# Kernel optimization log

Measured on AMD Instinct MI355X. Metric: run time of the kernel, lower is better.

The kernel has to match this reference:

```python
import jax, jax.numpy as jnp
import numpy as np

GRID = 12  # sqrt(144), seq_len = 144 fixed by w_g shape


def _relative_position(n: int) -> jnp.ndarray:
    # grid cell centers for an n x n grid, flattened row-major -> (n*n,)
    idx = np.arange(n * n)
    row, col = idx // n, idx % n
    cx = (col + 0.5) / n  # (x_min + x_max)/2 with x_min=col/n, x_max=(col+1)/n
    cy = (row + 0.5) / n
    dx = cx[:, None] - cx[None, :]
    dy = cy[:, None] - cy[None, :]
    ax = np.sign(dx) * 0.5
    ay = np.sign(dy) * 0.5
    dx = np.abs(np.log(np.abs(dx) + 0.5))
    dy = np.abs(np.log(np.abs(dy) + 0.5))
    # cat along leading dim then permute(1,2,0) == stack last-dim in order (dx,dy,ax,ay)
    pos = np.stack([dx, dy, ax, ay], axis=-1).astype(np.float32)  # (S,S,4)
    return jnp.asarray(pos)


def setup_inputs() -> dict:
    key = jax.random.key(0)
    ks = jax.random.split(key, 9)
    B, S, D = 128, GRID * GRID, 1024
    sc = 1.0 / np.sqrt(D)
    return {
        "query": jax.random.normal(ks[0], (B, S, D), jnp.float32),
        "key": jax.random.normal(ks[1], (B, S, D), jnp.float32),
        "value": jax.random.normal(ks[2], (B, S, D), jnp.float32),
        "Wq": jax.random.normal(ks[3], (D, D), jnp.float32) * sc,
        "bq": jnp.zeros((D,), jnp.float32),
        "Wk": jax.random.normal(ks[4], (D, D), jnp.float32) * sc,
        "bk": jnp.zeros((D,), jnp.float32),
        "Wv": jax.random.normal(ks[5], (D, D), jnp.float32) * sc,
        "bv": jnp.zeros((D,), jnp.float32),
        "Wlin": jax.random.normal(ks[6], (D, 4), jnp.float32) * 0.5,
        "w_g": jax.random.normal(ks[7], (S, D, 1), jnp.float32) * sc,
    }


def reference(query, key, value, Wq, bq, Wk, bk, Wv, bv, Wlin, w_g):
    d_model = query.shape[-1]
    # QKV projections + ReLU activation (dropout is identity at eval)
    q = jax.nn.relu(jnp.einsum("bsd,ed->bse", query, Wq) + bq)
    k = jax.nn.relu(jnp.einsum("bsd,ed->bse", key, Wk) + bk)
    v = jax.nn.relu(jnp.einsum("bsd,ed->bse", value, Wv) + bv)
    # raw scores: (B, S, S)
    att = jnp.einsum("bsd,btd->bst", q, k) * (d_model ** -0.5)
    # relative-position bias: (S, S, 4) -> linear -> relu -> per-row w_g -> relu
    pos = _relative_position(GRID)
    rp = jax.nn.relu(jnp.einsum("stf,df->std", pos, Wlin))  # (S, S, D)
    rp = jax.nn.relu(jnp.einsum("std,sdo->sto", rp, w_g)[..., 0])  # (S, S)
    att = jax.nn.softmax(att + rp[None, :, :], axis=-1)
    return jnp.einsum("bst,btd->bsd", att, v)
```

## Files before the change

kernel.cpp:

```cpp
#include <hip/hip_runtime.h>
#include <hip/hip_fp16.h>

#define DEV __device__ __forceinline__

using half8 = __attribute__((ext_vector_type(8))) _Float16;
using half4 = __attribute__((ext_vector_type(4))) _Float16;
using f32x4 = __attribute__((ext_vector_type(4))) float;

DEV void gload_lds16(const void* g, void* l) {
  __builtin_amdgcn_global_load_lds((const __attribute__((address_space(1))) unsigned int*)g,
                                   (__attribute__((address_space(3))) unsigned int*)l,
                                   16, 0, 0);
}

DEV f32x4 mfma16x32(half8 a, half8 b, f32x4 c) {
  return __builtin_amdgcn_mfma_f32_16x16x32_f16(a, b, c, 0, 0, 0);
}

__global__ void conv3_f32_f16(const float* __restrict__ s0, const float* __restrict__ s1,
                              const float* __restrict__ s2, _Float16* __restrict__ d0,
                              _Float16* __restrict__ d1, _Float16* __restrict__ d2, int n) {
  const float* s = blockIdx.z == 0 ? s0 : (blockIdx.z == 1 ? s1 : s2);
  _Float16* d = blockIdx.z == 0 ? d0 : (blockIdx.z == 1 ? d1 : d2);
  int i = (blockIdx.x * 256 + threadIdx.x) * 8;
  if (i >= n) return;
  float4 a = *(const float4*)(s + i);
  float4 b = *(const float4*)(s + i + 4);
  half8 h;
  h[0] = (_Float16)a.x; h[1] = (_Float16)a.y; h[2] = (_Float16)a.z; h[3] = (_Float16)a.w;
  h[4] = (_Float16)b.x; h[5] = (_Float16)b.y; h[6] = (_Float16)b.z; h[7] = (_Float16)b.w;
  *(half8*)(d + i) = h;
}

__global__ void vt_pad_zero(_Float16* __restrict__ vt) {
  int i = blockIdx.x * 256 + threadIdx.x;
  _Float16* p = vt + (size_t)i * 160 + 144;
  *(half8*)p = (half8){};
  *(half8*)(p + 8) = (half8){};
}

__global__ __launch_bounds__(192) void rp_kernel(const float* __restrict__ Wlin,
                                                 const float* __restrict__ wg,
                                                 float* __restrict__ rp) {
  int s = blockIdx.x, t = threadIdx.x;
  if (t >= 144) return;
  int rs = s / 12, cs = s % 12, rt = t / 12, ct = t % 12;
  float dx = (cs - ct) / 12.f, dy = (rs - rt) / 12.f;
  float ax = (dx > 0.f) ? 0.5f : (dx < 0.f ? -0.5f : 0.f);
  float ay = (dy > 0.f) ? 0.5f : (dy < 0.f ? -0.5f : 0.f);
  float lx = fabsf(logf(fabsf(dx) + 0.5f));
  float ly = fabsf(logf(fabsf(dy) + 0.5f));
  float a0 = 0.f, a1 = 0.f, a2 = 0.f, a3 = 0.f;
  const float* wgs = wg + s * 1024;
  for (int d = 0; d < 1024; d += 4) {
#pragma unroll
    for (int u = 0; u < 4; ++u) {
      float4 w = *(const float4*)(Wlin + (d + u) * 4);
      float dot = lx * w.x + ly * w.y + ax * w.z + ay * w.w;
      dot = dot > 0.f ? dot : 0.f;
      float p = dot * wgs[d + u];
      if (u == 0) a0 += p; else if (u == 1) a1 += p; else if (u == 2) a2 += p; else a3 += p;
    }
  }
  float acc = (a0 + a1) + (a2 + a3);
  rp[s * 144 + t] = acc > 0.f ? acc : 0.f;
}

__global__ __launch_bounds__(256, 2) void gemm_proj(
    const _Float16* __restrict__ a0q, const _Float16* __restrict__ a1q,
    const _Float16* __restrict__ a2q, const _Float16* __restrict__ w0q,
    const _Float16* __restrict__ w1q, const _Float16* __restrict__ w2q,
    const float* __restrict__ bi0, const float* __restrict__ bi1,
    const float* __restrict__ bi2, _Float16* __restrict__ c0q,
    _Float16* __restrict__ c1q, _Float16* __restrict__ c2q,
    _Float16* __restrict__ vtp, int vtz) {
  const _Float16* A = blockIdx.z == 0 ? a0q : (blockIdx.z == 1 ? a1q : a2q);
  const _Float16* W = blockIdx.z == 0 ? w0q : (blockIdx.z == 1 ? w1q : w2q);
  const float* bias = blockIdx.z == 0 ? bi0 : (blockIdx.z == 1 ? bi1 : bi2);
  _Float16* C = blockIdx.z == 0 ? c0q : (blockIdx.z == 1 ? c1q : c2q);

  __shared__ __align__(16) char lds[73728];
  int tid = threadIdx.x, wid = tid >> 6, lane = tid & 63;
  int lin = blockIdx.y * 8 + blockIdx.x;
  int local = lin >> 3;
  int mt = (lin & 7) * 9 + (local >> 3), nt = local & 7;
  int m0 = mt * 256, n0 = nt * 128;

  int r4l = lane >> 2, c4 = lane & 3;
  int cg8 = ((c4 + (r4l >> 1)) & 3) * 8;
  int lr = lane & 15, lg = lane >> 4;
  int rdoff = lr * 64 + ((lg - (lr >> 1)) & 3) * 16;

  const _Float16* gp[6];
#pragma unroll
  for (int c = 0; c < 6; ++c) {
    int q = c * 4 + wid;
    gp[c] = (q < 16) ? A + (size_t)(m0 + q * 16 + r4l) * 1024 + cg8
                     : W + (size_t)(n0 + (q - 16) * 16 + r4l) * 1024 + cg8;
  }
  char *sl0 = lds, *sl1 = lds + 24576, *sl2 = lds + 49152;
  auto issue = [&](char* slot) {
#pragma unroll
    for (int c = 0; c < 6; ++c) { gload_lds16(gp[c], slot + (c * 4 + wid) * 1024); gp[c] += 32; }
  };
  issue(sl0);
  issue(sl1);
  f32x4 acc[8][4] = {};
  int abase = (wid >> 1) * 8192, bbase = 16384 + (wid & 1) * 4096;
  for (int t = 0; t < 32; ++t) {
    asm volatile("s_waitcnt vmcnt(6)" ::: "memory");
    __builtin_amdgcn_s_barrier();
    __builtin_amdgcn_sched_barrier(0);
    issue(sl2);
    half8 a[8], b[4];
#pragma unroll
    for (int i = 0; i < 8; ++i) a[i] = *(const half8*)(sl0 + abase + i * 1024 + rdoff);
#pragma unroll
    for (int j = 0; j < 4; ++j) b[j] = *(const half8*)(sl0 + bbase + j * 1024 + rdoff);
#pragma unroll
    for (int i = 0; i < 8; ++i)
#pragma unroll
      for (int j = 0; j < 4; ++j)
        acc[i][j] = mfma16x32(b[j], a[i], acc[i][j]);
    char* tmp = sl0; sl0 = sl1; sl1 = sl2; sl2 = tmp;
  }
  int wm = (wid >> 1) * 128, wn = (wid & 1) * 64;
  bool tov = (vtp != nullptr) && ((int)blockIdx.z == vtz);
#pragma unroll
  for (int i = 0; i < 8; ++i) {
    int row = m0 + wm + i * 16 + lr;
#pragma unroll
    for (int j = 0; j < 4; ++j) {
      int col = n0 + wn + j * 16 + lg * 4;
      float4 b4 = *(const float4*)(bias + col);
      half4 h;
      float v0 = acc[i][j][0] + b4.x; h[0] = (_Float16)(v0 > 0.f ? v0 : 0.f);
      float v1 = acc[i][j][1] + b4.y; h[1] = (_Float16)(v1 > 0.f ? v1 : 0.f);
      float v2 = acc[i][j][2] + b4.z; h[2] = (_Float16)(v2 > 0.f ? v2 : 0.f);
      float v3 = acc[i][j][3] + b4.w; h[3] = (_Float16)(v3 > 0.f ? v3 : 0.f);
      if (tov) {
        int bb = row / 144, ss = row - bb * 144;
        _Float16* vb = vtp + (size_t)(bb * 1024 + col) * 160 + ss;
        vb[0] = h[0]; vb[160] = h[1]; vb[320] = h[2]; vb[480] = h[3];
      } else {
        *(half4*)(C + (size_t)row * 1024 + col) = h;
      }
    }
  }
}

__global__ __launch_bounds__(256) void attn_kernel(const _Float16* __restrict__ q,
                                                   const _Float16* __restrict__ k,
                                                   const _Float16* __restrict__ vt,
                                                   const float* __restrict__ rp,
                                                   float* __restrict__ out) {
  __shared__ __align__(16) char lds[53248];
  float* sc = (float*)lds;
  _Float16* P = (_Float16*)(lds + 36864);
  float* sums = (float*)(lds + 52992);

  int tid = threadIdx.x, wid = tid >> 6, lane = tid & 63;
  int lin = blockIdx.y * 3 + blockIdx.x;
  int swz = (lin & 7) * 48 + (lin >> 3);
  int mt3 = swz % 3, b = swz / 3;
  int m0 = mt3 * 48;
  const int nstart_t[4] = {0, 3, 5, 7};
  const int ncnt_t[4]   = {3, 2, 2, 2};
  int ns = nstart_t[wid], nc = ncnt_t[wid];
  int r4l = lane >> 2, c4 = lane & 3;
  int cg8 = ((c4 + (r4l >> 1)) & 3) * 8;
  int lr = lane & 15, lg = lane >> 4;
  int rdoff = lr * 64 + ((lg - (lr >> 1)) & 3) * 16;

  {
    char *sl0 = lds, *sl1 = lds + 12288, *sl2 = lds + 24576;
    const _Float16* g1[3];
#pragma unroll
    for (int c = 0; c < 3; ++c) {
      int qq = c * 4 + wid;
      g1[c] = (qq < 3) ? q + (size_t)(b * 144 + m0 + qq * 16 + r4l) * 1024 + cg8
                       : k + (size_t)(b * 144 + (qq - 3) * 16 + r4l) * 1024 + cg8;
    }
    auto issue1 = [&](char* slot) {
#pragma unroll
      for (int c = 0; c < 3; ++c) {
        gload_lds16(g1[c], slot + (c * 4 + wid) * 1024);
        g1[c] += 32;
      }
    };
    issue1(sl0);
    issue1(sl1);
    f32x4 acc[3][3] = {};
    for (int t = 0; t < 32; ++t) {
      asm volatile("s_waitcnt vmcnt(3)" ::: "memory");
      __builtin_amdgcn_sched_barrier(0);
      __builtin_amdgcn_s_barrier();
      __builtin_amdgcn_sched_barrier(0);
      issue1(sl2);
      half8 af[3], bf[3];
#pragma unroll
      for (int i = 0; i < 3; ++i)
        af[i] = *(const half8*)(sl0 + i * 1024 + rdoff);
#pragma unroll
      for (int j = 0; j < 3; ++j)
        if (j < nc)
          bf[j] = *(const half8*)(sl0 + (3 + ns + j) * 1024 + rdoff);
#pragma unroll
      for (int i = 0; i < 3; ++i)
#pragma unroll
        for (int j = 0; j < 3; ++j)
          if (j < nc)
            acc[i][j] = mfma16x32(bf[j], af[i], acc[i][j]);
      char* tmp = sl0; sl0 = sl1; sl1 = sl2; sl2 = tmp;
    }
    asm volatile("s_waitcnt vmcnt(0)" ::: "memory");
    __syncthreads();
    const float scale = 0.03125f;
#pragma unroll
    for (int i = 0; i < 3; ++i) {
      int qrow = i * 16 + lr;
#pragma unroll
      for (int j = 0; j < 3; ++j)
        if (j < nc) {
          int kc0 = (ns + j) * 16 + lg * 4;
          float4 rr = *(const float4*)(rp + (m0 + qrow) * 144 + kc0);
          f32x4 vs;
          vs[0] = acc[i][j][0] * scale + rr.x;
          vs[1] = acc[i][j][1] * scale + rr.y;
          vs[2] = acc[i][j][2] * scale + rr.z;
          vs[3] = acc[i][j][3] * scale + rr.w;
          *(f32x4*)(sc + qrow * 152 + kc0) = vs;
        }
    }
  }
  __syncthreads();

  if (tid < 192) {
    int r = tid >> 2, qd = tid & 3;
    int cb = qd * 36;
    float m = -1e30f;
    for (int c2 = 0; c2 < 36; ++c2) m = fmaxf(m, sc[r * 152 + cb + c2]);
    m = fmaxf(m, __shfl_xor(m, 1));
    m = fmaxf(m, __shfl_xor(m, 2));
    float s = 0.f;
    for (int c2 = 0; c2 < 36; ++c2) {
      float e = __expf(sc[r * 152 + cb + c2] - m);
      s += e;
      P[r * 168 + cb + c2] = (_Float16)e;
    }
    s += __shfl_xor(s, 1);
    s += __shfl_xor(s, 2);
    if (qd == 0) sums[r] = s;
  }
  if (tid < 96) {
    int r = tid >> 1, c0 = 144 + (tid & 1) * 8;
    *(half8*)(P + r * 168 + c0) = (half8){};
  }
  __syncthreads();

  char *s0p = lds, *s1p = lds + 16384;
  auto issue2 = [&](int idx, char* slot) {
    int nn0 = (idx / 5) * 256, kk0 = (idx % 5) * 32;
#pragma unroll
    for (int c = 0; c < 4; ++c) {
      int ch = c * 4 + wid;
      gload_lds16(vt + (size_t)(b * 1024 + nn0 + ch * 16 + r4l) * 160 + kk0 + cg8,
                  slot + ch * 1024);
    }
  };
  issue2(0, s0p);
  f32x4 o[3][4] = {};
  for (int it = 0; it < 20; ++it) {
    asm volatile("s_waitcnt vmcnt(0)" ::: "memory");
    __builtin_amdgcn_sched_barrier(0);
    __builtin_amdgcn_s_barrier();
    __builtin_amdgcn_sched_barrier(0);
    issue2(it + 1, ((it + 1) & 1) ? s1p : s0p);
    char* sb = (it & 1) ? s1p : s0p;
    int k0 = (it % 5) * 32;
    half8 af[3], bf[4];
#pragma unroll
    for (int i = 0; i < 3; ++i)
      af[i] = *(const half8*)(P + (i * 16 + lr) * 168 + k0 + lg * 8);
#pragma unroll
    for (int j = 0; j < 4; ++j)
      bf[j] = *(const half8*)(sb + (wid * 4 + j) * 1024 + rdoff);
#pragma unroll
    for (int i = 0; i < 3; ++i)
#pragma unroll
      for (int j = 0; j < 4; ++j)
        o[i][j] = mfma16x32(bf[j], af[i], o[i][j]);
    if (it % 5 == 4) {
      int n0 = (it / 5) * 256;
#pragma unroll
      for (int i = 0; i < 3; ++i) {
        int row = i * 16 + lr;
        float inv = 1.f / sums[row];
#pragma unroll
        for (int j = 0; j < 4; ++j) {
          f32x4 vo;
          vo[0] = o[i][j][0] * inv; vo[1] = o[i][j][1] * inv;
          vo[2] = o[i][j][2] * inv; vo[3] = o[i][j][3] * inv;
          *(f32x4*)(out + (size_t)(b * 144 + m0 + row) * 1024 + n0 + wid * 64 + j * 16 + lg * 4) = vo;
          o[i][j] = (f32x4){};
        }
      }
    }
  }
}

extern "C" void kernel_launch(void* const* d_in, const int* in_sizes, int n_in,
                              void* d_out, int out_size, void* d_ws, size_t ws_size,
                              hipStream_t stream) {
  const float* query = (const float*)d_in[0];
  const float* key   = (const float*)d_in[1];
  const float* value = (const float*)d_in[2];
  const float* Wq    = (const float*)d_in[3];
  const float* bq    = (const float*)d_in[4];
  const float* Wk    = (const float*)d_in[5];
  const float* bk    = (const float*)d_in[6];
  const float* Wv    = (const float*)d_in[7];
  const float* bv    = (const float*)d_in[8];
  const float* Wlin  = (const float*)d_in[9];
  const float* wg    = (const float*)d_in[10];
  float* out = (float*)d_out;

  char* ws = (char*)d_ws;
  const size_t NQKV = (size_t)18432 * 1024;
  const size_t NVT  = (size_t)131072 * 160;
  const int    NW   = 1024 * 1024;
  _Float16* Wqb = (_Float16*)(ws);
  _Float16* Wkb = (_Float16*)(ws + (2u << 20));
  _Float16* Wvb = (_Float16*)(ws + (4u << 20));
  float*    rp  = (float*)(ws + (6u << 20));
  _Float16* qp  = (_Float16*)(ws + (6u << 20) + 131072);
  _Float16* kp  = qp + NQKV;
  _Float16* vt  = kp + NQKV;

  dim3 agrid(3, 128);

  if (ws_size >= 238000000ull) {
    _Float16* ia = vt + NVT + 32768;
    _Float16* ib = ia + NQKV;
    _Float16* ic = ib + NQKV;
    conv3_f32_f16<<<dim3((int)(NQKV / 2048), 1, 3), 256, 0, stream>>>(
        query, key, value, ia, ib, ic, (int)NQKV);
    conv3_f32_f16<<<dim3(NW / 2048, 1, 3), 256, 0, stream>>>(Wq, Wk, Wv, Wqb, Wkb, Wvb, NW);
    rp_kernel<<<144, 192, 0, stream>>>(Wlin, wg, rp);
    vt_pad_zero<<<512, 256, 0, stream>>>(vt);
    gemm_proj<<<dim3(8, 72, 3), 256, 0, stream>>>(ia, ib, ic, Wqb, Wkb, Wvb,
                                                  bq, bk, bv, qp, kp, kp ,
                                                  vt, 2);
    attn_kernel<<<agrid, 256, 0, stream>>>(qp, kp, vt, rp, out);
  } else {
    _Float16* inb = vt + NVT;
    rp_kernel<<<144, 192, 0, stream>>>(Wlin, wg, rp);
    vt_pad_zero<<<512, 256, 0, stream>>>(vt);
    conv3_f32_f16<<<dim3(NW / 2048, 1, 3), 256, 0, stream>>>(Wq, Wk, Wv, Wqb, Wkb, Wvb, NW);
    conv3_f32_f16<<<dim3((int)(NQKV / 2048), 1, 1), 256, 0, stream>>>(
        query, query, query, inb, inb, inb, (int)NQKV);
    gemm_proj<<<dim3(8, 72, 1), 256, 0, stream>>>(inb, inb, inb, Wqb, Wqb, Wqb,
                                                  bq, bq, bq, qp, qp, qp, nullptr, -1);
    conv3_f32_f16<<<dim3((int)(NQKV / 2048), 1, 1), 256, 0, stream>>>(
        key, key, key, inb, inb, inb, (int)NQKV);
    gemm_proj<<<dim3(8, 72, 1), 256, 0, stream>>>(inb, inb, inb, Wkb, Wkb, Wkb,
                                                  bk, bk, bk, kp, kp, kp, nullptr, -1);
    conv3_f32_f16<<<dim3((int)(NQKV / 2048), 1, 1), 256, 0, stream>>>(
        value, value, value, inb, inb, inb, (int)NQKV);
    gemm_proj<<<dim3(8, 72, 1), 256, 0, stream>>>(inb, inb, inb, Wvb, Wvb, Wvb,
                                                  bv, bv, bv, qp , qp, qp,
                                                  vt, 0);
    attn_kernel<<<agrid, 256, 0, stream>>>(qp, kp, vt, rp, out);
  }
}
```

Before: 319.3 us.

## Fuse fp32-to-fp16 activation conversion into the projection GEMM load path

The projection GEMM now streams fp32 query/key/value tiles directly into LDS and converts them to fp16 in registers with packed round-toward-zero conversions before the MFMAs. This removes the separate conversion kernel and its full read-write pass over the three activation tensors. To fit the doubled A-tile bytes in the same LDS budget, the M tile shrinks from 256 to 128 rows with a new swizzle, and the grid doubles. The fallback path for small workspace is removed, since the fp16 activation staging buffers are no longer needed. In exchange, the GEMM reads twice as many bytes per A element and does less MFMA work per loaded B tile. The conversion mode also changes from default rounding to round-toward-zero.

```diff
diff --git a/kernel.cpp b/kernel.cpp
--- a/kernel.cpp
+++ b/kernel.cpp
@@ -5,6 +5,8 @@
 
 using half8 = __attribute__((ext_vector_type(8))) _Float16;
 using half4 = __attribute__((ext_vector_type(4))) _Float16;
+using half2v = __attribute__((ext_vector_type(2))) _Float16;
+using fp16x2 = __attribute__((ext_vector_type(2))) __fp16;
 using f32x4 = __attribute__((ext_vector_type(4))) float;
 
 DEV void gload_lds16(const void* g, void* l) {
@@ -15,6 +17,16 @@
 
 DEV f32x4 mfma16x32(half8 a, half8 b, f32x4 c) {
   return __builtin_amdgcn_mfma_f32_16x16x32_f16(a, b, c, 0, 0, 0);
+}
+
+DEV half8 cvt8(f32x4 lo, f32x4 hi) {
+  half2v p0 = __builtin_bit_cast(half2v, __builtin_amdgcn_cvt_pkrtz(lo[0], lo[1]));
+  half2v p1 = __builtin_bit_cast(half2v, __builtin_amdgcn_cvt_pkrtz(lo[2], lo[3]));
+  half2v p2 = __builtin_bit_cast(half2v, __builtin_amdgcn_cvt_pkrtz(hi[0], hi[1]));
+  half2v p3 = __builtin_bit_cast(half2v, __builtin_amdgcn_cvt_pkrtz(hi[2], hi[3]));
+  half4 q0 = __builtin_shufflevector(p0, p1, 0, 1, 2, 3);
+  half4 q1 = __builtin_shufflevector(p2, p3, 0, 1, 2, 3);
+  return __builtin_shufflevector(q0, q1, 0, 1, 2, 3, 4, 5, 6, 7);
 }
 
 __global__ void conv3_f32_f16(const float* __restrict__ s0, const float* __restrict__ s1,
@@ -67,14 +79,14 @@
 }
 
 __global__ __launch_bounds__(256, 2) void gemm_proj(
-    const _Float16* __restrict__ a0q, const _Float16* __restrict__ a1q,
-    const _Float16* __restrict__ a2q, const _Float16* __restrict__ w0q,
+    const float* __restrict__ A0, const float* __restrict__ A1,
+    const float* __restrict__ A2, const _Float16* __restrict__ w0q,
     const _Float16* __restrict__ w1q, const _Float16* __restrict__ w2q,
     const float* __restrict__ bi0, const float* __restrict__ bi1,
     const float* __restrict__ bi2, _Float16* __restrict__ c0q,
     _Float16* __restrict__ c1q, _Float16* __restrict__ c2q,
     _Float16* __restrict__ vtp, int vtz) {
-  const _Float16* A = blockIdx.z == 0 ? a0q : (blockIdx.z == 1 ? a1q : a2q);
+  const float* A = blockIdx.z == 0 ? A0 : (blockIdx.z == 1 ? A1 : A2);
   const _Float16* W = blockIdx.z == 0 ? w0q : (blockIdx.z == 1 ? w1q : w2q);
   const float* bias = blockIdx.z == 0 ? bi0 : (blockIdx.z == 1 ? bi1 : bi2);
   _Float16* C = blockIdx.z == 0 ? c0q : (blockIdx.z == 1 ? c1q : c2q);
@@ -83,51 +95,72 @@
   int tid = threadIdx.x, wid = tid >> 6, lane = tid & 63;
   int lin = blockIdx.y * 8 + blockIdx.x;
   int local = lin >> 3;
-  int mt = (lin & 7) * 9 + (local >> 3), nt = local & 7;
-  int m0 = mt * 256, n0 = nt * 128;
+  int mt = (lin & 7) * 18 + (local >> 3), nt = local & 7;
+  int m0 = mt * 128, n0 = nt * 128;
 
   int r4l = lane >> 2, c4 = lane & 3;
   int cg8 = ((c4 + (r4l >> 1)) & 3) * 8;
   int lr = lane & 15, lg = lane >> 4;
   int rdoff = lr * 64 + ((lg - (lr >> 1)) & 3) * 16;
-
-  const _Float16* gp[6];
-#pragma unroll
-  for (int c = 0; c < 6; ++c) {
-    int q = c * 4 + wid;
-    gp[c] = (q < 16) ? A + (size_t)(m0 + q * 16 + r4l) * 1024 + cg8
-                     : W + (size_t)(n0 + (q - 16) * 16 + r4l) * 1024 + cg8;
-  }
+  int ar = lane >> 3, ac = lane & 7;
+  int acs = ((ac + ar) & 7) * 4;
+  int rr = lr & 7, sub = lr >> 3;
+  int s0off = rr * 128 + (((2 * lg - rr) & 7) << 4);
+  int s1off = rr * 128 + (((2 * lg + 1 - rr) & 7) << 4);
+
+  const float* gpA[4];
+#pragma unroll
+  for (int c = 0; c < 4; ++c)
+    gpA[c] = A + (size_t)(m0 + (c * 4 + wid) * 8 + ar) * 1024 + acs;
+  const _Float16* gpB[2];
+#pragma unroll
+  for (int c = 0; c < 2; ++c)
+    gpB[c] = W + (size_t)(n0 + (c * 4 + wid) * 16 + r4l) * 1024 + cg8;
+
   char *sl0 = lds, *sl1 = lds + 24576, *sl2 = lds + 49152;
   auto issue = [&](char* slot) {
 #pragma unroll
-    for (int c = 0; c < 6; ++c) { gload_lds16(gp[c], slot + (c * 4 + wid) * 1024); gp[c] += 32; }
+    for (int c = 0; c < 4; ++c) { gload_lds16(gpA[c], slot + (c * 4 + wid) * 1024); gpA[c] += 32; }
+#pragma unroll
+    for (int c = 0; c < 2; ++c) { gload_lds16(gpB[c], slot + 16384 + (c * 4 + wid) * 1024); gpB[c] += 32; }
   };
   issue(sl0);
   issue(sl1);
-  f32x4 acc[8][4] = {};
-  int abase = (wid >> 1) * 8192, bbase = 16384 + (wid & 1) * 4096;
+  f32x4 acc[4][4] = {};
+  int wm = (wid >> 1) * 64, wn = (wid & 1) * 64;
+  int achunk0 = wm >> 3, bchunk0 = wn >> 4;
   for (int t = 0; t < 32; ++t) {
     asm volatile("s_waitcnt vmcnt(6)" ::: "memory");
     __builtin_amdgcn_s_barrier();
     __builtin_amdgcn_sched_barrier(0);
     issue(sl2);
-    half8 a[8], b[4];
-#pragma unroll
-    for (int i = 0; i < 8; ++i) a[i] = *(const half8*)(sl0 + abase + i * 1024 + rdoff);
-#pragma unroll
-    for (int j = 0; j < 4; ++j) b[j] = *(const half8*)(sl0 + bbase + j * 1024 + rdoff);
-#pragma unroll
-    for (int i = 0; i < 8; ++i)
+    if (t == 29) {
+#pragma unroll
+      for (int c = 0; c < 4; ++c) gpA[c] -= 64;
+#pragma unroll
+      for (int c = 0; c < 2; ++c) gpB[c] -= 64;
+    }
+    half8 a[4], b[4];
+#pragma unroll
+    for (int i = 0; i < 4; ++i) {
+      const char* ab = sl0 + (achunk0 + i * 2 + sub) * 1024;
+      f32x4 lo = *(const f32x4*)(ab + s0off);
+      f32x4 hi = *(const f32x4*)(ab + s1off);
+      a[i] = cvt8(lo, hi);
+    }
+#pragma unroll
+    for (int j = 0; j < 4; ++j)
+      b[j] = *(const half8*)(sl0 + 16384 + (bchunk0 + j) * 1024 + rdoff);
+#pragma unroll
+    for (int i = 0; i < 4; ++i)
 #pragma unroll
       for (int j = 0; j < 4; ++j)
         acc[i][j] = mfma16x32(b[j], a[i], acc[i][j]);
     char* tmp = sl0; sl0 = sl1; sl1 = sl2; sl2 = tmp;
   }
-  int wm = (wid >> 1) * 128, wn = (wid & 1) * 64;
   bool tov = (vtp != nullptr) && ((int)blockIdx.z == vtz);
 #pragma unroll
-  for (int i = 0; i < 8; ++i) {
+  for (int i = 0; i < 4; ++i) {
     int row = m0 + wm + i * 16 + lr;
 #pragma unroll
     for (int j = 0; j < 4; ++j) {
@@ -333,43 +366,17 @@
   _Float16* Wkb = (_Float16*)(ws + (2u << 20));
   _Float16* Wvb = (_Float16*)(ws + (4u << 20));
   float*    rp  = (float*)(ws + (6u << 20));
-  _Float16* qp  = (_Float16*)(ws + (6u << 20) + 131072);
+  _Float16* vt  = (_Float16*)(ws + (6u << 20) + 131072);
+  _Float16* qp  = vt + NVT;
   _Float16* kp  = qp + NQKV;
-  _Float16* vt  = kp + NQKV;
 
   dim3 agrid(3, 128);
 
-  if (ws_size >= 238000000ull) {
-    _Float16* ia = vt + NVT + 32768;
-    _Float16* ib = ia + NQKV;
-    _Float16* ic = ib + NQKV;
-    conv3_f32_f16<<<dim3((int)(NQKV / 2048), 1, 3), 256, 0, stream>>>(
-        query, key, value, ia, ib, ic, (int)NQKV);
-    conv3_f32_f16<<<dim3(NW / 2048, 1, 3), 256, 0, stream>>>(Wq, Wk, Wv, Wqb, Wkb, Wvb, NW);
-    rp_kernel<<<144, 192, 0, stream>>>(Wlin, wg, rp);
-    vt_pad_zero<<<512, 256, 0, stream>>>(vt);
-    gemm_proj<<<dim3(8, 72, 3), 256, 0, stream>>>(ia, ib, ic, Wqb, Wkb, Wvb,
-                                                  bq, bk, bv, qp, kp, kp ,
-                                                  vt, 2);
-    attn_kernel<<<agrid, 256, 0, stream>>>(qp, kp, vt, rp, out);
-  } else {
-    _Float16* inb = vt + NVT;
-    rp_kernel<<<144, 192, 0, stream>>>(Wlin, wg, rp);
-    vt_pad_zero<<<512, 256, 0, stream>>>(vt);
-    conv3_f32_f16<<<dim3(NW / 2048, 1, 3), 256, 0, stream>>>(Wq, Wk, Wv, Wqb, Wkb, Wvb, NW);
-    conv3_f32_f16<<<dim3((int)(NQKV / 2048), 1, 1), 256, 0, stream>>>(
-        query, query, query, inb, inb, inb, (int)NQKV);
-    gemm_proj<<<dim3(8, 72, 1), 256, 0, stream>>>(inb, inb, inb, Wqb, Wqb, Wqb,
-                                                  bq, bq, bq, qp, qp, qp, nullptr, -1);
-    conv3_f32_f16<<<dim3((int)(NQKV / 2048), 1, 1), 256, 0, stream>>>(
-        key, key, key, inb, inb, inb, (int)NQKV);
-    gemm_proj<<<dim3(8, 72, 1), 256, 0, stream>>>(inb, inb, inb, Wkb, Wkb, Wkb,
-                                                  bk, bk, bk, kp, kp, kp, nullptr, -1);
-    conv3_f32_f16<<<dim3((int)(NQKV / 2048), 1, 1), 256, 0, stream>>>(
-        value, value, value, inb, inb, inb, (int)NQKV);
-    gemm_proj<<<dim3(8, 72, 1), 256, 0, stream>>>(inb, inb, inb, Wvb, Wvb, Wvb,
-                                                  bv, bv, bv, qp , qp, qp,
-                                                  vt, 0);
-    attn_kernel<<<agrid, 256, 0, stream>>>(qp, kp, vt, rp, out);
-  }
-}
+  conv3_f32_f16<<<dim3(NW / 2048, 1, 3), 256, 0, stream>>>(Wq, Wk, Wv, Wqb, Wkb, Wvb, NW);
+  rp_kernel<<<144, 192, 0, stream>>>(Wlin, wg, rp);
+  vt_pad_zero<<<512, 256, 0, stream>>>(vt);
+  gemm_proj<<<dim3(8, 144, 3), 256, 0, stream>>>(query, key, value, Wqb, Wkb, Wvb,
+                                                 bq, bk, bv, qp, kp, kp ,
+                                                 vt, 2);
+  attn_kernel<<<agrid, 256, 0, stream>>>(qp, kp, vt, rp, out);
+}
```

Result: slower. 340.0 us (+6.5%).

## Overlap K/V fp32-to-fp16 conversion with Q projection GEMM in one launch

Applied to the files above, without the earlier changes.

Only the query input is converted to fp16 up front. A new kernel interleaves Q-projection GEMM blocks (every third block) with blocks that convert the key and value inputs, so memory-bound conversion runs alongside compute-bound GEMM work. A second launch then runs the K and V projections. The low-workspace fallback path is removed and the workspace layout changes, which assumes a large workspace is always available.

```diff
diff --git a/kernel.cpp b/kernel.cpp
--- a/kernel.cpp
+++ b/kernel.cpp
@@ -17,19 +17,24 @@
   return __builtin_amdgcn_mfma_f32_16x16x32_f16(a, b, c, 0, 0, 0);
 }
 
-__global__ void conv3_f32_f16(const float* __restrict__ s0, const float* __restrict__ s1,
-                              const float* __restrict__ s2, _Float16* __restrict__ d0,
-                              _Float16* __restrict__ d1, _Float16* __restrict__ d2, int n) {
-  const float* s = blockIdx.z == 0 ? s0 : (blockIdx.z == 1 ? s1 : s2);
-  _Float16* d = blockIdx.z == 0 ? d0 : (blockIdx.z == 1 ? d1 : d2);
-  int i = (blockIdx.x * 256 + threadIdx.x) * 8;
-  if (i >= n) return;
+DEV void conv2048(const float* __restrict__ s, _Float16* __restrict__ d, int tid) {
+  int i = tid * 8;
   float4 a = *(const float4*)(s + i);
   float4 b = *(const float4*)(s + i + 4);
   half8 h;
   h[0] = (_Float16)a.x; h[1] = (_Float16)a.y; h[2] = (_Float16)a.z; h[3] = (_Float16)a.w;
   h[4] = (_Float16)b.x; h[5] = (_Float16)b.y; h[6] = (_Float16)b.z; h[7] = (_Float16)b.w;
   *(half8*)(d + i) = h;
+}
+
+__global__ void conv3_f32_f16(const float* __restrict__ s0, const float* __restrict__ s1,
+                              const float* __restrict__ s2, _Float16* __restrict__ d0,
+                              _Float16* __restrict__ d1, _Float16* __restrict__ d2, int n) {
+  const float* s = blockIdx.z == 0 ? s0 : (blockIdx.z == 1 ? s1 : s2);
+  _Float16* d = blockIdx.z == 0 ? d0 : (blockIdx.z == 1 ? d1 : d2);
+  int i = blockIdx.x * 2048;
+  if (i >= n) return;
+  conv2048(s + i, d + i, (int)threadIdx.x);
 }
 
 __global__ void vt_pad_zero(_Float16* __restrict__ vt) {
@@ -66,22 +71,10 @@
   rp[s * 144 + t] = acc > 0.f ? acc : 0.f;
 }
 
-__global__ __launch_bounds__(256, 2) void gemm_proj(
-    const _Float16* __restrict__ a0q, const _Float16* __restrict__ a1q,
-    const _Float16* __restrict__ a2q, const _Float16* __restrict__ w0q,
-    const _Float16* __restrict__ w1q, const _Float16* __restrict__ w2q,
-    const float* __restrict__ bi0, const float* __restrict__ bi1,
-    const float* __restrict__ bi2, _Float16* __restrict__ c0q,
-    _Float16* __restrict__ c1q, _Float16* __restrict__ c2q,
-    _Float16* __restrict__ vtp, int vtz) {
-  const _Float16* A = blockIdx.z == 0 ? a0q : (blockIdx.z == 1 ? a1q : a2q);
-  const _Float16* W = blockIdx.z == 0 ? w0q : (blockIdx.z == 1 ? w1q : w2q);
-  const float* bias = blockIdx.z == 0 ? bi0 : (blockIdx.z == 1 ? bi1 : bi2);
-  _Float16* C = blockIdx.z == 0 ? c0q : (blockIdx.z == 1 ? c1q : c2q);
-
-  __shared__ __align__(16) char lds[73728];
+DEV void gemm_body(char* lds, int lin, const _Float16* __restrict__ A,
+                   const _Float16* __restrict__ W, const float* __restrict__ bias,
+                   _Float16* __restrict__ C, _Float16* __restrict__ vtp) {
   int tid = threadIdx.x, wid = tid >> 6, lane = tid & 63;
-  int lin = blockIdx.y * 8 + blockIdx.x;
   int local = lin >> 3;
   int mt = (lin & 7) * 9 + (local >> 3), nt = local & 7;
   int m0 = mt * 256, n0 = nt * 128;
@@ -125,7 +118,7 @@
     char* tmp = sl0; sl0 = sl1; sl1 = sl2; sl2 = tmp;
   }
   int wm = (wid >> 1) * 128, wn = (wid & 1) * 64;
-  bool tov = (vtp != nullptr) && ((int)blockIdx.z == vtz);
+  bool tov = (vtp != nullptr);
 #pragma unroll
   for (int i = 0; i < 8; ++i) {
     int row = m0 + wm + i * 16 + lr;
@@ -149,6 +142,39 @@
   }
 }
 
+__global__ __launch_bounds__(256, 2) void gemm_q_conv_kv(
+    const _Float16* __restrict__ ia, const _Float16* __restrict__ Wqb,
+    const float* __restrict__ bq, _Float16* __restrict__ qp,
+    const float* __restrict__ key, const float* __restrict__ value,
+    _Float16* __restrict__ ib, _Float16* __restrict__ ic) {
+  __shared__ __align__(16) char lds[73728];
+  int id = blockIdx.x;
+  if (id % 3 == 0) {
+    gemm_body(lds, id / 3, ia, Wqb, bq, qp, nullptr);
+  } else {
+    int cid = id - id / 3 - 1;
+    const size_t NQ = (size_t)18432 * 1024;
+    size_t base = (size_t)cid * 32768;
+#pragma unroll
+    for (int it = 0; it < 16; ++it) {
+      size_t e = base + (size_t)it * 2048;
+      if (e < NQ) conv2048(key + e, ib + e, (int)threadIdx.x);
+      else        conv2048(value + (e - NQ), ic + (e - NQ), (int)threadIdx.x);
+    }
+  }
+}
+
+__global__ __launch_bounds__(256, 2) void gemm_kv(
+    const _Float16* __restrict__ ib, const _Float16* __restrict__ ic,
+    const _Float16* __restrict__ Wkb, const _Float16* __restrict__ Wvb,
+    const float* __restrict__ bk, const float* __restrict__ bv,
+    _Float16* __restrict__ kp, _Float16* __restrict__ vt) {
+  __shared__ __align__(16) char lds[73728];
+  int lin = blockIdx.y * 8 + blockIdx.x;
+  if (blockIdx.z == 0) gemm_body(lds, lin, ib, Wkb, bk, kp, nullptr);
+  else                 gemm_body(lds, lin, ic, Wvb, bv, kp , vt);
+}
+
 __global__ __launch_bounds__(256) void attn_kernel(const _Float16* __restrict__ q,
                                                    const _Float16* __restrict__ k,
                                                    const _Float16* __restrict__ vt,
@@ -333,43 +359,21 @@
   _Float16* Wkb = (_Float16*)(ws + (2u << 20));
   _Float16* Wvb = (_Float16*)(ws + (4u << 20));
   float*    rp  = (float*)(ws + (6u << 20));
-  _Float16* qp  = (_Float16*)(ws + (6u << 20) + 131072);
-  _Float16* kp  = qp + NQKV;
-  _Float16* vt  = kp + NQKV;
+  _Float16* ia  = (_Float16*)(ws + (6u << 20) + 131072);
+  _Float16* ib  = ia + NQKV;
+  _Float16* ic  = ib + NQKV;
+  _Float16* vt  = ic + NQKV;
+  _Float16* kp  = vt + NVT;
+  _Float16* qp  = kp + NQKV;
 
   dim3 agrid(3, 128);
 
-  if (ws_size >= 238000000ull) {
-    _Float16* ia = vt + NVT + 32768;
-    _Float16* ib = ia + NQKV;
-    _Float16* ic = ib + NQKV;
-    conv3_f32_f16<<<dim3((int)(NQKV / 2048), 1, 3), 256, 0, stream>>>(
-        query, key, value, ia, ib, ic, (int)NQKV);
-    conv3_f32_f16<<<dim3(NW / 2048, 1, 3), 256, 0, stream>>>(Wq, Wk, Wv, Wqb, Wkb, Wvb, NW);
-    rp_kernel<<<144, 192, 0, stream>>>(Wlin, wg, rp);
-    vt_pad_zero<<<512, 256, 0, stream>>>(vt);
-    gemm_proj<<<dim3(8, 72, 3), 256, 0, stream>>>(ia, ib, ic, Wqb, Wkb, Wvb,
-                                                  bq, bk, bv, qp, kp, kp ,
-                                                  vt, 2);
-    attn_kernel<<<agrid, 256, 0, stream>>>(qp, kp, vt, rp, out);
-  } else {
-    _Float16* inb = vt + NVT;
-    rp_kernel<<<144, 192, 0, stream>>>(Wlin, wg, rp);
-    vt_pad_zero<<<512, 256, 0, stream>>>(vt);
-    conv3_f32_f16<<<dim3(NW / 2048, 1, 3), 256, 0, stream>>>(Wq, Wk, Wv, Wqb, Wkb, Wvb, NW);
-    conv3_f32_f16<<<dim3((int)(NQKV / 2048), 1, 1), 256, 0, stream>>>(
-        query, query, query, inb, inb, inb, (int)NQKV);
-    gemm_proj<<<dim3(8, 72, 1), 256, 0, stream>>>(inb, inb, inb, Wqb, Wqb, Wqb,
-                                                  bq, bq, bq, qp, qp, qp, nullptr, -1);
-    conv3_f32_f16<<<dim3((int)(NQKV / 2048), 1, 1), 256, 0, stream>>>(
-        key, key, key, inb, inb, inb, (int)NQKV);
-    gemm_proj<<<dim3(8, 72, 1), 256, 0, stream>>>(inb, inb, inb, Wkb, Wkb, Wkb,
-                                                  bk, bk, bk, kp, kp, kp, nullptr, -1);
-    conv3_f32_f16<<<dim3((int)(NQKV / 2048), 1, 1), 256, 0, stream>>>(
-        value, value, value, inb, inb, inb, (int)NQKV);
-    gemm_proj<<<dim3(8, 72, 1), 256, 0, stream>>>(inb, inb, inb, Wvb, Wvb, Wvb,
-                                                  bv, bv, bv, qp , qp, qp,
-                                                  vt, 0);
-    attn_kernel<<<agrid, 256, 0, stream>>>(qp, kp, vt, rp, out);
-  }
-}
+  conv3_f32_f16<<<dim3((int)(NQKV / 2048), 1, 1), 256, 0, stream>>>(
+      query, query, query, ia, ia, ia, (int)NQKV);
+  conv3_f32_f16<<<dim3(NW / 2048, 1, 3), 256, 0, stream>>>(Wq, Wk, Wv, Wqb, Wkb, Wvb, NW);
+  rp_kernel<<<144, 192, 0, stream>>>(Wlin, wg, rp);
+  vt_pad_zero<<<512, 256, 0, stream>>>(vt);
+  gemm_q_conv_kv<<<1728, 256, 0, stream>>>(ia, Wqb, bq, qp, key, value, ib, ic);
+  gemm_kv<<<dim3(8, 72, 2), 256, 0, stream>>>(ib, ic, Wkb, Wvb, bk, bv, kp, vt);
+  attn_kernel<<<agrid, 256, 0, stream>>>(qp, kp, vt, rp, out);
+}
```

Result: slower. 340.2 us (+6.5%).
